# Optimization experiments

Measured on AMD Instinct MI355X. Metric: run time of the kernel, lower is better.

The kernel has to match this reference:

```python
import jax, jax.numpy as jnp
import numpy as np

N_NODES = 100000
N_EDGES = 1600000
IN_FEATS = 128
N_HIDDEN = 128
N_CLASSES = 64


def setup_inputs() -> dict:
    key = jax.random.key(0)
    ks = jax.random.split(key, 12)
    features = jax.random.normal(ks[0], (N_NODES, IN_FEATS), dtype=jnp.float32)
    src = jax.random.randint(ks[1], (N_EDGES,), 0, N_NODES, dtype=jnp.int32)
    dst = jax.random.randint(ks[2], (N_EDGES,), 0, N_NODES, dtype=jnp.int32)
    def lin(k, fi, fo):
        s = 1.0 / np.sqrt(fi)
        kw, kb = jax.random.split(k)
        W = jax.random.uniform(kw, (fi, fo), jnp.float32, -s, s)
        b = jax.random.uniform(kb, (fo,), jnp.float32, -s, s)
        return W, b
    W1, b1 = lin(ks[3], IN_FEATS, N_HIDDEN)
    W2a, b2a = lin(ks[4], N_HIDDEN, N_HIDDEN)
    W2b, b2b = lin(ks[5], N_HIDDEN, N_HIDDEN)
    W3, b3 = lin(ks[6], N_HIDDEN, N_CLASSES)
    eps = jnp.zeros((4,), jnp.float32)  # learnable eps, one per GINConv
    return dict(features=features, src=src, dst=dst, W1=W1, b1=b1,
                W2a=W2a, b2a=b2a, W2b=W2b, b2b=b2b, W3=W3, b3=b3, eps=eps)


def _aggregate(h, src, dst, mode, deg):
    # messages flow src -> dst; h[src] is [E, d]
    msg = h[src]
    if mode == 'sum':
        return jax.ops.segment_sum(msg, dst, num_segments=N_NODES)
    if mode == 'mean':
        s = jax.ops.segment_sum(msg, dst, num_segments=N_NODES)
        return s / jnp.maximum(deg, 1.0)[:, None]
    # max: DGL yields 0 for nodes with no incoming edges
    m = jax.ops.segment_max(msg, dst, num_segments=N_NODES)
    return jnp.where(deg[:, None] > 0, m, 0.0)


def reference(features, src, dst, W1, b1, W2a, b2a, W2b, b2b, W3, b3, eps):
    deg = jax.ops.segment_sum(jnp.ones((N_EDGES,), jnp.float32), dst,
                              num_segments=N_NODES)
    h = features
    # layer 0: max aggregation + Linear + ReLU (dropout = identity in eval)
    h = (1.0 + eps[0]) * h + _aggregate(h, src, dst, 'max', deg)
    h = jax.nn.relu(h @ W1 + b1)
    # middle layers: sum aggregation + Linear + ReLU
    h = (1.0 + eps[1]) * h + _aggregate(h, src, dst, 'sum', deg)
    h = jax.nn.relu(h @ W2a + b2a)
    h = (1.0 + eps[2]) * h + _aggregate(h, src, dst, 'sum', deg)
    h = jax.nn.relu(h @ W2b + b2b)
    # output layer: mean aggregation + Linear (no activation)
    h = (1.0 + eps[3]) * h + _aggregate(h, src, dst, 'mean', deg)
    h = h @ W3 + b3
    return h
```

## Files before the change

### kernel.cpp

```cpp
#include <hip/hip_runtime.h>
#include <math.h>

#define N_NODES 100000
#define N_EDGES 1600000
#define FEAT 128
#define NBUCKET 391
#define BCAP 5120

typedef __attribute__((ext_vector_type(8))) _Float16 half8;
typedef __attribute__((ext_vector_type(4))) float floatx4;

__device__ inline half8 h8max(half8 a, half8 b) {
    return __builtin_elementwise_max(a, b);
}

__global__ __launch_bounds__(256) void zero_i32(int* p, int n) {
    int i = blockIdx.x * 256 + threadIdx.x;
    if (i < n) p[i] = 0;
}

__global__ __launch_bounds__(512) void bin_edges(const int* __restrict__ src,
                                                 const int* __restrict__ dst,
                                                 uint2* __restrict__ ebuf,
                                                 int* __restrict__ gcur) {
    __shared__ int hist[NBUCKET];
    __shared__ int lbase[NBUCKET];
    __shared__ int cur[NBUCKET];
    __shared__ uint2 tile[4096];

    int t = threadIdx.x;
    int e0 = blockIdx.x * 4096;
    for (int i = t; i < NBUCKET; i += 512) { hist[i] = 0; cur[i] = 0; }
    __syncthreads();

    for (int i = t; i < 4096; i += 512) {
        int e = e0 + i;
        uint2 v; v.x = 0u; v.y = 0xffffffffu;
        if (e < N_EDGES) { v.x = (unsigned)src[e]; v.y = (unsigned)dst[e]; }
        tile[i] = v;
        if (v.y != 0xffffffffu) atomicAdd(&hist[v.y >> 8], 1);
    }
    __syncthreads();

    for (int i = t; i < NBUCKET; i += 512) {
        int c = hist[i];
        lbase[i] = (c > 0) ? atomicAdd(&gcur[i], c) : 0;
    }
    __syncthreads();

    for (int i = t; i < 4096; i += 512) {
        uint2 v = tile[i];
        if (v.y == 0xffffffffu) continue;
        int b = (int)(v.y >> 8);
        int p = lbase[b] + atomicAdd(&cur[b], 1);
        if (p < BCAP) ebuf[(size_t)b * BCAP + p] = v;
    }
}

__global__ __launch_bounds__(512) void scan_buckets(const int* __restrict__ gcur,
                                                    int* __restrict__ bbase,
                                                    int* __restrict__ rowptr) {
    __shared__ int s[512];
    int t = threadIdx.x;
    int v = (t < NBUCKET) ? gcur[t] : 0;
    s[t] = v;
    __syncthreads();
    for (int off = 1; off < 512; off <<= 1) {
        int u = (t >= off) ? s[t - off] : 0;
        __syncthreads();
        s[t] += u;
        __syncthreads();
    }
    if (t < NBUCKET) bbase[t] = s[t] - v;
    if (t == 0) rowptr[N_NODES] = N_EDGES;
}

__global__ __launch_bounds__(256) void bucket_csr(const uint2* __restrict__ ebuf,
                                                  const int* __restrict__ gcur,
                                                  const int* __restrict__ bbase,
                                                  int* __restrict__ rowptr,
                                                  int* __restrict__ esrc) {
    __shared__ int cnt[256];
    __shared__ int off[256];
    __shared__ int astart[256];
    __shared__ int cur[256];

    int b = blockIdx.x, t = threadIdx.x;
    int total = gcur[b]; if (total > BCAP) total = BCAP;
    int base = bbase[b];
    const uint2* eb = ebuf + (size_t)b * BCAP;

    cnt[t] = 0; cur[t] = 0;
    __syncthreads();
    for (int i = t; i < total; i += 256) atomicAdd(&cnt[eb[i].y & 255], 1);
    __syncthreads();

    int v = cnt[t];
    off[t] = v;
    __syncthreads();
    for (int o = 1; o < 256; o <<= 1) {
        int u = (t >= o) ? off[t - o] : 0;
        __syncthreads();
        off[t] += u;
        __syncthreads();
    }
    int excl = off[t] - v;
    int node = (b << 8) + t;
    if (node < N_NODES) rowptr[node] = base + excl;
    astart[t] = base + excl;
    __syncthreads();

    for (int i = t; i < total; i += 256) {
        uint2 e = eb[i];
        int ln = (int)(e.y & 255);
        int p = astart[ln] + atomicAdd(&cur[ln], 1);
        esrc[p] = (int)e.x;
    }
}

__global__ __launch_bounds__(256) void f32_to_f16_vec(const float* __restrict__ in,
                                                      _Float16* __restrict__ out,
                                                      int n4) {
    int i = blockIdx.x * 256 + threadIdx.x;
    int stride = gridDim.x * 256;
    for (; i < n4; i += stride) {
        float4 v = ((const float4*)in)[i];
        union { uint2 u; _Float16 h[4]; } p;
        p.h[0] = (_Float16)v.x; p.h[1] = (_Float16)v.y;
        p.h[2] = (_Float16)v.z; p.h[3] = (_Float16)v.w;
        *(uint2*)(out + 4 * (size_t)i) = p.u;
    }
}

__global__ __launch_bounds__(256) void wprep(const float* __restrict__ W,
                                             _Float16* __restrict__ WT,
                                             int K, int N) {
    int idx = blockIdx.x * 256 + threadIdx.x;
    if (idx < K * N) {
        int n = idx / K, k = idx % K;
        WT[idx] = (_Float16)W[k * N + n];
    }
}

template <int MODE, int D, bool OUTF32, bool BIAS>
__global__ __launch_bounds__(256) void agg_kernel(const _Float16* __restrict__ h,
                                                  const int* __restrict__ rowptr,
                                                  const int* __restrict__ esrc,
                                                  const float* __restrict__ eps,
                                                  int ei,
                                                  const float* __restrict__ bias,
                                                  _Float16* __restrict__ outH,
                                                  float* __restrict__ outF) {
    constexpr int LPE = D / 8;
    constexpr int NPW = 64 / LPE;
    int wid = (int)((blockIdx.x * 256 + threadIdx.x) >> 6);
    int l = threadIdx.x & 63;
    int grp = l / LPE, sl = l % LPE;
    int node = wid * NPW + grp;
    if (node >= N_NODES) return;
    int beg = rowptr[node], end = rowptr[node + 1];
    int deg = end - beg;

    const _Float16 NEUT = (MODE == 0) ? (_Float16)(-65504.0f) : (_Float16)(0.0f);
    half8 neut8 = {NEUT, NEUT, NEUT, NEUT, NEUT, NEUT, NEUT, NEUT};
    half8 acc = neut8;

    for (int e = beg; e < end; e += 8) {
        half8 v[8];
#pragma unroll
        for (int j = 0; j < 8; ++j) {
            int ee = e + j;
            int s = esrc[ee < end ? ee : end - 1];
            v[j] = *(const half8*)(h + (size_t)s * D + sl * 8);
        }
#pragma unroll
        for (int j = 0; j < 8; ++j)
            if (e + j >= end) v[j] = neut8;
        if (MODE == 0) {
            half8 m01 = h8max(v[0], v[1]), m23 = h8max(v[2], v[3]);
            half8 m45 = h8max(v[4], v[5]), m67 = h8max(v[6], v[7]);
            acc = h8max(acc, h8max(h8max(m01, m23), h8max(m45, m67)));
        } else {
            half8 s01 = v[0] + v[1], s23 = v[2] + v[3];
            half8 s45 = v[4] + v[5], s67 = v[6] + v[7];
            acc += (s01 + s23) + (s45 + s67);
        }
    }

    float a[8];
#pragma unroll
    for (int i = 0; i < 8; ++i) a[i] = (float)acc[i];
    if (MODE == 0 && deg == 0) {
#pragma unroll
        for (int i = 0; i < 8; ++i) a[i] = 0.f;
    }
    if (MODE == 2) {
        float inv = 1.f / (float)(deg > 0 ? deg : 1);
#pragma unroll
        for (int i = 0; i < 8; ++i) a[i] *= inv;
    }
    float sc = 1.f + eps[ei];
    half8 self = *(const half8*)(h + (size_t)node * D + sl * 8);
    float o[8];
#pragma unroll
    for (int i = 0; i < 8; ++i) o[i] = fmaf(sc, (float)self[i], a[i]);

    if (OUTF32) {
#pragma unroll
        for (int i = 0; i < 8; ++i)
            if (BIAS) o[i] += bias[sl * 8 + i];
        float4* dstp = (float4*)(outF + (size_t)node * D + sl * 8);
        dstp[0] = make_float4(o[0], o[1], o[2], o[3]);
        dstp[1] = make_float4(o[4], o[5], o[6], o[7]);
    } else {
        half8 ov;
#pragma unroll
        for (int i = 0; i < 8; ++i) ov[i] = (_Float16)o[i];
        *(half8*)(outH + (size_t)node * D + sl * 8) = ov;
    }
}

template <int BN, bool RELU, bool BIAS>
__global__ __launch_bounds__(256) void gemm_mfma(const _Float16* __restrict__ X,
                                                 const _Float16* __restrict__ WT,
                                                 const float* __restrict__ bias,
                                                 _Float16* __restrict__ Yh) {
    __shared__ _Float16 Xs[64 * 128];
    __shared__ _Float16 Ws[BN * 128];
    char* xb = (char*)Xs;
    char* wb = (char*)Ws;

    int t = threadIdx.x;
    int l = t & 63, w = t >> 6;
    int lr = l & 15, lg = l >> 4;
    int rowBase = blockIdx.x * 64;

    {
        int row = t >> 2, q = t & 3;
        int grow = rowBase + row;
        const char* srcp = (const char*)(X + (size_t)grow * 128) + q * 64;
#pragma unroll
        for (int j = 0; j < 4; ++j) {
            int byte = q * 64 + j * 16;
            half8 v = {};
            if (grow < N_NODES) v = *(const half8*)(srcp + j * 16);
            *(half8*)(xb + row * 256 + (byte ^ ((row & 7) << 4))) = v;
        }
    }
    {
#pragma unroll
        for (int p = 0; p < BN / 16; ++p) {
            int idx = p * 4096 + t * 16;
            int row = idx >> 8, byte = idx & 255;
            *(half8*)(wb + row * 256 + (byte ^ ((row & 7) << 4))) =
                *(const half8*)((const char*)WT + idx);
        }
    }
    __syncthreads();

    constexpr int NCT = BN / 16;
    floatx4 acc[NCT];
#pragma unroll
    for (int ct = 0; ct < NCT; ++ct)
#pragma unroll
        for (int r = 0; r < 4; ++r) acc[ct][r] = 0.f;

#pragma unroll
    for (int ks = 0; ks < 4; ++ks) {
        int kbyte = ks * 64 + lg * 16;
        int r = w * 16 + lr;
        half8 a = *(const half8*)(xb + r * 256 + (kbyte ^ ((r & 7) << 4)));
#pragma unroll
        for (int ct = 0; ct < NCT; ++ct) {
            int n = ct * 16 + lr;
            half8 b = *(const half8*)(wb + n * 256 + (kbyte ^ ((n & 7) << 4)));
            acc[ct] = __builtin_amdgcn_mfma_f32_16x16x32_f16(a, b, acc[ct], 0, 0, 0);
        }
    }

    float bv[NCT];
#pragma unroll
    for (int ct = 0; ct < NCT; ++ct) bv[ct] = BIAS ? bias[ct * 16 + lr] : 0.f;

    constexpr int ROWB = BN * 2;
    __syncthreads();
#pragma unroll
    for (int ct = 0; ct < NCT; ++ct)
#pragma unroll
        for (int r = 0; r < 4; ++r) {
            int row = w * 16 + lg * 4 + r;
            int col = ct * 16 + lr;
            float v = acc[ct][r] + bv[ct];
            if (RELU) v = fmaxf(v, 0.f);
            *(_Float16*)(xb + row * ROWB + ((col * 2) ^ ((row & 7) << 4))) =
                (_Float16)v;
        }
    __syncthreads();
    {
        int row = t >> 2, q = t & 3;
        int grow = rowBase + row;
        if (grow < N_NODES) {
            char* dstp = (char*)(Yh + (size_t)grow * BN) + q * (ROWB / 4);
#pragma unroll
            for (int j = 0; j < ROWB / 64; ++j) {
                int byte = q * (ROWB / 4) + j * 16;
                half8 v = *(const half8*)(xb + row * ROWB + (byte ^ ((row & 7) << 4)));
                *(half8*)(dstp + j * 16) = v;
            }
        }
    }
}

extern "C" void kernel_launch(void* const* d_in, const int* in_sizes, int n_in,
                              void* d_out, int out_size, void* d_ws, size_t ws_size,
                              hipStream_t stream) {
    const float* feat = (const float*)d_in[0];
    const int*   src  = (const int*)d_in[1];
    const int*   dst  = (const int*)d_in[2];
    const float* W1   = (const float*)d_in[3];
    const float* b1   = (const float*)d_in[4];
    const float* W2a  = (const float*)d_in[5];
    const float* b2a  = (const float*)d_in[6];
    const float* W2b  = (const float*)d_in[7];
    const float* b2b  = (const float*)d_in[8];
    const float* W3   = (const float*)d_in[9];
    const float* b3   = (const float*)d_in[10];
    const float* eps  = (const float*)d_in[11];

    const size_t NH = (size_t)N_NODES * FEAT;
    char* base = (char*)d_ws;
    auto alloc = [&](size_t bytes) {
        char* p = base;
        base += (bytes + 255) & ~(size_t)255;
        return p;
    };
    _Float16* featH = (_Float16*)alloc(NH * 2);
    _Float16* hA    = (_Float16*)alloc(NH * 2);
    _Float16* hB    = (_Float16*)alloc(NH * 2);
    _Float16* WT1   = (_Float16*)alloc(128 * 128 * 2);
    _Float16* WT2a  = (_Float16*)alloc(128 * 128 * 2);
    _Float16* WT2b  = (_Float16*)alloc(128 * 128 * 2);
    _Float16* WT3   = (_Float16*)alloc(128 * 64 * 2);
    uint2* ebuf     = (uint2*)alloc((size_t)NBUCKET * BCAP * 8);
    int* rowptr     = (int*)alloc((N_NODES + 1) * 4);
    int* esrc       = (int*)alloc((size_t)N_EDGES * 4);
    int* gcur       = (int*)alloc(NBUCKET * 4);
    int* bbase      = (int*)alloc(NBUCKET * 4);

    f32_to_f16_vec<<<2048, 256, 0, stream>>>(feat, featH, (int)(NH / 4));
    wprep<<<64, 256, 0, stream>>>(W1, WT1, 128, 128);
    wprep<<<64, 256, 0, stream>>>(W2a, WT2a, 128, 128);
    wprep<<<64, 256, 0, stream>>>(W2b, WT2b, 128, 128);
    wprep<<<32, 256, 0, stream>>>(W3, WT3, 128, 64);

    zero_i32<<<(NBUCKET + 255) / 256, 256, 0, stream>>>(gcur, NBUCKET);
    bin_edges<<<(N_EDGES + 4095) / 4096, 512, 0, stream>>>(src, dst, ebuf, gcur);
    scan_buckets<<<1, 512, 0, stream>>>(gcur, bbase, rowptr);
    bucket_csr<<<NBUCKET, 256, 0, stream>>>(ebuf, gcur, bbase, rowptr, esrc);

    const int AGG128_GRID = (N_NODES + 15) / 16;
    const int AGG64_GRID  = (N_NODES + 31) / 32;
    const int GEMM_GRID = (N_NODES + 63) / 64;

    agg_kernel<0, 128, false, false><<<AGG128_GRID, 256, 0, stream>>>(
        featH, rowptr, esrc, eps, 0, nullptr, hB, nullptr);
    gemm_mfma<128, true, true><<<GEMM_GRID, 256, 0, stream>>>(hB, WT1, b1, hA);
    agg_kernel<1, 128, false, false><<<AGG128_GRID, 256, 0, stream>>>(
        hA, rowptr, esrc, eps, 1, nullptr, hB, nullptr);
    gemm_mfma<128, true, true><<<GEMM_GRID, 256, 0, stream>>>(hB, WT2a, b2a, hA);
    agg_kernel<1, 128, false, false><<<AGG128_GRID, 256, 0, stream>>>(
        hA, rowptr, esrc, eps, 2, nullptr, hB, nullptr);
    gemm_mfma<128, true, true><<<GEMM_GRID, 256, 0, stream>>>(hB, WT2b, b2b, hA);
    gemm_mfma<64, false, false><<<GEMM_GRID, 256, 0, stream>>>(hA, WT3, nullptr, hB);
    agg_kernel<2, 64, true, true><<<AGG64_GRID, 256, 0, stream>>>(
        hB, rowptr, esrc, eps, 3, b3, nullptr, (float*)d_out);
}
```

Before: 342.1 us.

## Fuse neighbor aggregation with MFMA linear layer for first three GIN layers

Adds a fused kernel that aggregates neighbor features for a 64-node tile into swizzled shared memory, then runs a 128x128 MFMA GEMM with bias and ReLU on that tile and writes fp16 output. This replaces three agg+gemm kernel pairs, removing the intermediate write and re-read of the aggregated hidden state plus three launches. In exchange each block loads the full 32KB weight matrix into LDS, uses 48KB of shared memory, which can limit occupancy during the latency-bound gather phase. Each block also aggregates only 64 nodes with 16-lane groups per node, so gather parallelism may differ from the old aggregation kernel.

```diff
diff --git a/kernel.cpp b/kernel.cpp
--- a/kernel.cpp
+++ b/kernel.cpp
@@ -139,6 +139,133 @@
     if (idx < K * N) {
         int n = idx / K, k = idx % K;
         WT[idx] = (_Float16)W[k * N + n];
+    }
+}
+
+template <int MODE, bool RELU>
+__global__ __launch_bounds__(256) void fused_agg_gemm(const _Float16* __restrict__ h,
+                                                      const int* __restrict__ rowptr,
+                                                      const int* __restrict__ esrc,
+                                                      const float* __restrict__ eps,
+                                                      int ei,
+                                                      const _Float16* __restrict__ WT,
+                                                      const float* __restrict__ bias,
+                                                      _Float16* __restrict__ Yh) {
+    __shared__ _Float16 Xs[64 * 128];
+    __shared__ _Float16 Ws[128 * 128];
+    char* xb = (char*)Xs;
+    char* wb = (char*)Ws;
+
+    int t = threadIdx.x;
+    int l = t & 63, w = t >> 6;
+    int lr = l & 15, lg = l >> 4;
+    int rowBase = blockIdx.x * 64;
+
+#pragma unroll
+    for (int p = 0; p < 8; ++p) {
+        int idx = p * 4096 + t * 16;
+        int row = idx >> 8, byte = idx & 255;
+        *(half8*)(wb + row * 256 + (byte ^ ((row & 7) << 4))) =
+            *(const half8*)((const char*)WT + idx);
+    }
+
+    float sc = 1.f + eps[ei];
+    const _Float16 NEUT = (MODE == 0) ? (_Float16)(-65504.0f) : (_Float16)(0.0f);
+    half8 neut8 = {NEUT, NEUT, NEUT, NEUT, NEUT, NEUT, NEUT, NEUT};
+
+    for (int sub = 0; sub < 4; ++sub) {
+        int rloc = w * 16 + sub * 4 + lg;
+        int node = rowBase + rloc;
+        half8 ov = {};
+        if (node < N_NODES) {
+            int beg = rowptr[node], end = rowptr[node + 1];
+            int deg = end - beg;
+            half8 acc = neut8;
+            for (int e = beg; e < end; e += 8) {
+                half8 v[8];
+#pragma unroll
+                for (int j = 0; j < 8; ++j) {
+                    int ee = e + j;
+                    int s = esrc[ee < end ? ee : end - 1];
+                    v[j] = *(const half8*)(h + (size_t)s * FEAT + lr * 8);
+                }
+#pragma unroll
+                for (int j = 0; j < 8; ++j)
+                    if (e + j >= end) v[j] = neut8;
+                if (MODE == 0) {
+                    half8 m01 = h8max(v[0], v[1]), m23 = h8max(v[2], v[3]);
+                    half8 m45 = h8max(v[4], v[5]), m67 = h8max(v[6], v[7]);
+                    acc = h8max(acc, h8max(h8max(m01, m23), h8max(m45, m67)));
+                } else {
+                    half8 s01 = v[0] + v[1], s23 = v[2] + v[3];
+                    half8 s45 = v[4] + v[5], s67 = v[6] + v[7];
+                    acc += (s01 + s23) + (s45 + s67);
+                }
+            }
+            float a[8];
+#pragma unroll
+            for (int i = 0; i < 8; ++i) a[i] = (float)acc[i];
+            if (MODE == 0 && deg == 0) {
+#pragma unroll
+                for (int i = 0; i < 8; ++i) a[i] = 0.f;
+            }
+            half8 self = *(const half8*)(h + (size_t)node * FEAT + lr * 8);
+#pragma unroll
+            for (int i = 0; i < 8; ++i)
+                ov[i] = (_Float16)fmaf(sc, (float)self[i], a[i]);
+        }
+        *(half8*)(xb + rloc * 256 + ((lr * 16) ^ ((rloc & 7) << 4))) = ov;
+    }
+    __syncthreads();
+
+    floatx4 acc[8];
+#pragma unroll
+    for (int ct = 0; ct < 8; ++ct)
+#pragma unroll
+        for (int r = 0; r < 4; ++r) acc[ct][r] = 0.f;
+
+#pragma unroll
+    for (int ks = 0; ks < 4; ++ks) {
+        int kbyte = ks * 64 + lg * 16;
+        int r = w * 16 + lr;
+        half8 a = *(const half8*)(xb + r * 256 + (kbyte ^ ((r & 7) << 4)));
+#pragma unroll
+        for (int ct = 0; ct < 8; ++ct) {
+            int n = ct * 16 + lr;
+            half8 b = *(const half8*)(wb + n * 256 + (kbyte ^ ((n & 7) << 4)));
+            acc[ct] = __builtin_amdgcn_mfma_f32_16x16x32_f16(a, b, acc[ct], 0, 0, 0);
+        }
+    }
+
+    float bv[8];
+#pragma unroll
+    for (int ct = 0; ct < 8; ++ct) bv[ct] = bias[ct * 16 + lr];
+
+    __syncthreads();
+#pragma unroll
+    for (int ct = 0; ct < 8; ++ct)
+#pragma unroll
+        for (int r = 0; r < 4; ++r) {
+            int row = w * 16 + lg * 4 + r;
+            int col = ct * 16 + lr;
+            float v = acc[ct][r] + bv[ct];
+            if (RELU) v = fmaxf(v, 0.f);
+            *(_Float16*)(xb + row * 256 + ((col * 2) ^ ((row & 7) << 4))) =
+                (_Float16)v;
+        }
+    __syncthreads();
+    {
+        int row = t >> 2, q = t & 3;
+        int grow = rowBase + row;
+        if (grow < N_NODES) {
+            char* dstp = (char*)(Yh + (size_t)grow * 128) + q * 64;
+#pragma unroll
+            for (int j = 0; j < 4; ++j) {
+                int byte = q * 64 + j * 16;
+                half8 v = *(const half8*)(xb + row * 256 + (byte ^ ((row & 7) << 4)));
+                *(half8*)(dstp + j * 16) = v;
+            }
+        }
     }
 }
 
@@ -358,19 +485,16 @@
     scan_buckets<<<1, 512, 0, stream>>>(gcur, bbase, rowptr);
     bucket_csr<<<NBUCKET, 256, 0, stream>>>(ebuf, gcur, bbase, rowptr, esrc);
 
-    const int AGG128_GRID = (N_NODES + 15) / 16;
-    const int AGG64_GRID  = (N_NODES + 31) / 32;
-    const int GEMM_GRID = (N_NODES + 63) / 64;
-
-    agg_kernel<0, 128, false, false><<<AGG128_GRID, 256, 0, stream>>>(
-        featH, rowptr, esrc, eps, 0, nullptr, hB, nullptr);
-    gemm_mfma<128, true, true><<<GEMM_GRID, 256, 0, stream>>>(hB, WT1, b1, hA);
-    agg_kernel<1, 128, false, false><<<AGG128_GRID, 256, 0, stream>>>(
-        hA, rowptr, esrc, eps, 1, nullptr, hB, nullptr);
-    gemm_mfma<128, true, true><<<GEMM_GRID, 256, 0, stream>>>(hB, WT2a, b2a, hA);
-    agg_kernel<1, 128, false, false><<<AGG128_GRID, 256, 0, stream>>>(
-        hA, rowptr, esrc, eps, 2, nullptr, hB, nullptr);
-    gemm_mfma<128, true, true><<<GEMM_GRID, 256, 0, stream>>>(hB, WT2b, b2b, hA);
+    const int FUSED_GRID = (N_NODES + 63) / 64;
+    const int AGG64_GRID = (N_NODES + 31) / 32;
+    const int GEMM_GRID  = (N_NODES + 63) / 64;
+
+    fused_agg_gemm<0, true><<<FUSED_GRID, 256, 0, stream>>>(
+        featH, rowptr, esrc, eps, 0, WT1, b1, hA);
+    fused_agg_gemm<1, true><<<FUSED_GRID, 256, 0, stream>>>(
+        hA, rowptr, esrc, eps, 1, WT2a, b2a, hB);
+    fused_agg_gemm<1, true><<<FUSED_GRID, 256, 0, stream>>>(
+        hB, rowptr, esrc, eps, 2, WT2b, b2b, hA);
     gemm_mfma<64, false, false><<<GEMM_GRID, 256, 0, stream>>>(hA, WT3, nullptr, hB);
     agg_kernel<2, 64, true, true><<<AGG64_GRID, 256, 0, stream>>>(
         hB, rowptr, esrc, eps, 3, b3, nullptr, (float*)d_out);
```

Measured after the change: 329.4 us. 1.04x faster.

## Fuse prep kernels and load GEMM A fragments directly from global

Applied to the files above, without the earlier changes.

The feature fp16 conversion, the four weight transposes and the bucket-counter zeroing now run in one kernel instead of six launches. The MFMA GEMM no longer stages the X tile in shared memory. Each lane reads its A fragment straight from global memory, and the weight buffer is reused for output staging. This cuts launch overhead and LDS footprint, which may raise occupancy, at the cost of less coalesced, uncached-in-LDS global reads for A.

```diff
diff --git a/kernel.cpp b/kernel.cpp
--- a/kernel.cpp
+++ b/kernel.cpp
@@ -14,9 +14,37 @@
     return __builtin_elementwise_max(a, b);
 }
 
-__global__ __launch_bounds__(256) void zero_i32(int* p, int n) {
-    int i = blockIdx.x * 256 + threadIdx.x;
-    if (i < n) p[i] = 0;
+__global__ __launch_bounds__(256) void prep_all(const float* __restrict__ feat,
+                                                _Float16* __restrict__ featH,
+                                                const float* __restrict__ W1,
+                                                const float* __restrict__ W2a,
+                                                const float* __restrict__ W2b,
+                                                const float* __restrict__ W3,
+                                                _Float16* __restrict__ WT1,
+                                                _Float16* __restrict__ WT2a,
+                                                _Float16* __restrict__ WT2b,
+                                                _Float16* __restrict__ WT3,
+                                                int* __restrict__ gcur) {
+    const int n4 = (N_NODES * FEAT) / 4;
+    int idx = blockIdx.x * 256 + threadIdx.x;
+    if (idx < n4) {
+        float4 v = ((const float4*)feat)[idx];
+        union { uint2 u; _Float16 h[4]; } p;
+        p.h[0] = (_Float16)v.x; p.h[1] = (_Float16)v.y;
+        p.h[2] = (_Float16)v.z; p.h[3] = (_Float16)v.w;
+        *(uint2*)(featH + 4 * (size_t)idx) = p.u;
+        return;
+    }
+    int off = idx - n4;
+    if (off < 16384) { int n = off / 128, k = off % 128; WT1[off] = (_Float16)W1[k * 128 + n]; return; }
+    off -= 16384;
+    if (off < 16384) { int n = off / 128, k = off % 128; WT2a[off] = (_Float16)W2a[k * 128 + n]; return; }
+    off -= 16384;
+    if (off < 16384) { int n = off / 128, k = off % 128; WT2b[off] = (_Float16)W2b[k * 128 + n]; return; }
+    off -= 16384;
+    if (off < 8192)  { int n = off / 128, k = off % 128; WT3[off] = (_Float16)W3[k * 64 + n]; return; }
+    off -= 8192;
+    if (off < NBUCKET) gcur[off] = 0;
 }
 
 __global__ __launch_bounds__(512) void bin_edges(const int* __restrict__ src,
@@ -115,30 +143,6 @@
         int ln = (int)(e.y & 255);
         int p = astart[ln] + atomicAdd(&cur[ln], 1);
         esrc[p] = (int)e.x;
-    }
-}
-
-__global__ __launch_bounds__(256) void f32_to_f16_vec(const float* __restrict__ in,
-                                                      _Float16* __restrict__ out,
-                                                      int n4) {
-    int i = blockIdx.x * 256 + threadIdx.x;
-    int stride = gridDim.x * 256;
-    for (; i < n4; i += stride) {
-        float4 v = ((const float4*)in)[i];
-        union { uint2 u; _Float16 h[4]; } p;
-        p.h[0] = (_Float16)v.x; p.h[1] = (_Float16)v.y;
-        p.h[2] = (_Float16)v.z; p.h[3] = (_Float16)v.w;
-        *(uint2*)(out + 4 * (size_t)i) = p.u;
-    }
-}
-
-__global__ __launch_bounds__(256) void wprep(const float* __restrict__ W,
-                                             _Float16* __restrict__ WT,
-                                             int K, int N) {
-    int idx = blockIdx.x * 256 + threadIdx.x;
-    if (idx < K * N) {
-        int n = idx / K, k = idx % K;
-        WT[idx] = (_Float16)W[k * N + n];
     }
 }
 
@@ -225,9 +229,7 @@
                                                  const _Float16* __restrict__ WT,
                                                  const float* __restrict__ bias,
                                                  _Float16* __restrict__ Yh) {
-    __shared__ _Float16 Xs[64 * 128];
     __shared__ _Float16 Ws[BN * 128];
-    char* xb = (char*)Xs;
     char* wb = (char*)Ws;
 
     int t = threadIdx.x;
@@ -235,26 +237,12 @@
     int lr = l & 15, lg = l >> 4;
     int rowBase = blockIdx.x * 64;
 
-    {
-        int row = t >> 2, q = t & 3;
-        int grow = rowBase + row;
-        const char* srcp = (const char*)(X + (size_t)grow * 128) + q * 64;
-#pragma unroll
-        for (int j = 0; j < 4; ++j) {
-            int byte = q * 64 + j * 16;
-            half8 v = {};
-            if (grow < N_NODES) v = *(const half8*)(srcp + j * 16);
-            *(half8*)(xb + row * 256 + (byte ^ ((row & 7) << 4))) = v;
-        }
-    }
-    {
-#pragma unroll
-        for (int p = 0; p < BN / 16; ++p) {
-            int idx = p * 4096 + t * 16;
-            int row = idx >> 8, byte = idx & 255;
-            *(half8*)(wb + row * 256 + (byte ^ ((row & 7) << 4))) =
-                *(const half8*)((const char*)WT + idx);
-        }
+#pragma unroll
+    for (int p = 0; p < BN / 16; ++p) {
+        int idx = p * 4096 + t * 16;
+        int row = idx >> 8, byte = idx & 255;
+        *(half8*)(wb + row * 256 + (byte ^ ((row & 7) << 4))) =
+            *(const half8*)((const char*)WT + idx);
     }
     __syncthreads();
 
@@ -265,15 +253,17 @@
 #pragma unroll
         for (int r = 0; r < 4; ++r) acc[ct][r] = 0.f;
 
+    int grow = rowBase + w * 16 + lr;
+    int arow = grow < N_NODES ? grow : 0;
+    const char* xrow = (const char*)(X + (size_t)arow * 128);
+
 #pragma unroll
     for (int ks = 0; ks < 4; ++ks) {
-        int kbyte = ks * 64 + lg * 16;
-        int r = w * 16 + lr;
-        half8 a = *(const half8*)(xb + r * 256 + (kbyte ^ ((r & 7) << 4)));
+        half8 a = *(const half8*)(xrow + ks * 64 + lg * 16);
 #pragma unroll
         for (int ct = 0; ct < NCT; ++ct) {
             int n = ct * 16 + lr;
-            half8 b = *(const half8*)(wb + n * 256 + (kbyte ^ ((n & 7) << 4)));
+            half8 b = *(const half8*)(wb + n * 256 + ((ks * 64 + lg * 16) ^ ((n & 7) << 4)));
             acc[ct] = __builtin_amdgcn_mfma_f32_16x16x32_f16(a, b, acc[ct], 0, 0, 0);
         }
     }
@@ -292,19 +282,19 @@
             int col = ct * 16 + lr;
             float v = acc[ct][r] + bv[ct];
             if (RELU) v = fmaxf(v, 0.f);
-            *(_Float16*)(xb + row * ROWB + ((col * 2) ^ ((row & 7) << 4))) =
+            *(_Float16*)(wb + row * ROWB + ((col * 2) ^ ((row & 7) << 4))) =
                 (_Float16)v;
         }
     __syncthreads();
     {
         int row = t >> 2, q = t & 3;
-        int grow = rowBase + row;
-        if (grow < N_NODES) {
-            char* dstp = (char*)(Yh + (size_t)grow * BN) + q * (ROWB / 4);
+        int g2 = rowBase + row;
+        if (g2 < N_NODES) {
+            char* dstp = (char*)(Yh + (size_t)g2 * BN) + q * (ROWB / 4);
 #pragma unroll
             for (int j = 0; j < ROWB / 64; ++j) {
                 int byte = q * (ROWB / 4) + j * 16;
-                half8 v = *(const half8*)(xb + row * ROWB + (byte ^ ((row & 7) << 4)));
+                half8 v = *(const half8*)(wb + row * ROWB + (byte ^ ((row & 7) << 4)));
                 *(half8*)(dstp + j * 16) = v;
             }
         }
@@ -347,20 +337,17 @@
     int* gcur       = (int*)alloc(NBUCKET * 4);
     int* bbase      = (int*)alloc(NBUCKET * 4);
 
-    f32_to_f16_vec<<<2048, 256, 0, stream>>>(feat, featH, (int)(NH / 4));
-    wprep<<<64, 256, 0, stream>>>(W1, WT1, 128, 128);
-    wprep<<<64, 256, 0, stream>>>(W2a, WT2a, 128, 128);
-    wprep<<<64, 256, 0, stream>>>(W2b, WT2b, 128, 128);
-    wprep<<<32, 256, 0, stream>>>(W3, WT3, 128, 64);
-
-    zero_i32<<<(NBUCKET + 255) / 256, 256, 0, stream>>>(gcur, NBUCKET);
+    const int PREP_ITEMS = (int)(NH / 4) + 16384 * 3 + 8192 + NBUCKET;
+    prep_all<<<(PREP_ITEMS + 255) / 256, 256, 0, stream>>>(
+        feat, featH, W1, W2a, W2b, W3, WT1, WT2a, WT2b, WT3, gcur);
+
     bin_edges<<<(N_EDGES + 4095) / 4096, 512, 0, stream>>>(src, dst, ebuf, gcur);
     scan_buckets<<<1, 512, 0, stream>>>(gcur, bbase, rowptr);
     bucket_csr<<<NBUCKET, 256, 0, stream>>>(ebuf, gcur, bbase, rowptr, esrc);
 
     const int AGG128_GRID = (N_NODES + 15) / 16;
     const int AGG64_GRID  = (N_NODES + 31) / 32;
-    const int GEMM_GRID = (N_NODES + 63) / 64;
+    const int GEMM_GRID   = (N_NODES + 63) / 64;
 
     agg_kernel<0, 128, false, false><<<AGG128_GRID, 256, 0, stream>>>(
         featH, rowptr, esrc, eps, 0, nullptr, hB, nullptr);
```

New measurement: 325.6 us. 4.8% less time.
